# Kernel tuning notes

Measured on AMD Instinct MI355X. Metric: run time of the kernel, lower is better.

The kernel has to match this reference:

```python
import jax, jax.numpy as jnp
import numpy as np

D_MODEL = 1024
NUM_HEADS = 16
HEAD_DIM = D_MODEL // NUM_HEADS


def setup_inputs() -> dict:
    key = jax.random.key(0)
    k_x, k_wqkv, k_bqkv, k_wout, k_bout = jax.random.split(key, 5)
    B, S = 2, 2048
    x = jax.random.normal(k_x, (B, S, D_MODEL), dtype=jnp.float32)
    # haiku Linear: y = x @ W + b, W shape [in, out]
    init_scale = 1.0 / np.sqrt(D_MODEL)
    W_qkv = jax.random.normal(k_wqkv, (D_MODEL, 3 * D_MODEL), dtype=jnp.float32) * init_scale
    b_qkv = jnp.zeros((3 * D_MODEL,), dtype=jnp.float32)
    W_out = jax.random.normal(k_wout, (D_MODEL, D_MODEL), dtype=jnp.float32) * init_scale
    b_out = jnp.zeros((D_MODEL,), dtype=jnp.float32)
    return {"x": x, "W_qkv": W_qkv, "b_qkv": b_qkv, "W_out": W_out, "b_out": b_out}


def reference(x, W_qkv, b_qkv, W_out, b_out):
    B, S, _ = x.shape
    qkv = x @ W_qkv + b_qkv                      # [B, S, 3*D]
    q, k, v = jnp.split(qkv, 3, axis=-1)         # each [B, S, D]
    # [B, S, D] -> [B, H, S, Hd]
    def heads(t):
        return t.reshape(B, S, NUM_HEADS, HEAD_DIM).transpose(0, 2, 1, 3)
    q, k, v = heads(q), heads(k), heads(v)
    scale = jnp.sqrt(jnp.float32(HEAD_DIM)).astype(x.dtype)
    attn = jnp.einsum('bhqd,bhkd->bhqk', q, k) / scale   # [B, H, S, S]
    attn = jax.nn.softmax(attn, axis=-1)
    out = jnp.einsum('bhqk,bhkd->bhqd', attn, v)          # [B, H, S, Hd]
    out = out.transpose(0, 2, 1, 3).reshape(B, S, D_MODEL)
    return out @ W_out + b_out
```

## Files before the change

kernel.cpp:

```cpp
#include <hip/hip_runtime.h>
#include <stdint.h>


#define BATCH 2
#define SEQ 2048
#define DM 1024
#define NH 16
#define HD 64
#define M_TOT 4096
#define QSCALE 0.18033688011112042f

typedef __bf16 bf16x8 __attribute__((ext_vector_type(8)));
typedef __bf16 bf16x4 __attribute__((ext_vector_type(4)));
typedef float  f32x4  __attribute__((ext_vector_type(4)));

__device__ __forceinline__ void gld_lds16(const void* g, void* l) {
    __builtin_amdgcn_global_load_lds(
        (const __attribute__((address_space(1))) uint32_t*)g,
        (__attribute__((address_space(3))) uint32_t*)l, 16, 0, 0);
}

__device__ __forceinline__ int swz(int r, int c) {
    return r * 64 + ((((c >> 3) ^ (r & 7))) << 3) + (c & 7);
}

__launch_bounds__(256)
__global__ void prep_kernel(const float* __restrict__ x,
                            const float* __restrict__ Wqkv,
                            const float* __restrict__ Wout,
                            __bf16* __restrict__ xs,
                            __bf16* __restrict__ wqt,
                            __bf16* __restrict__ wot)
{
    __shared__ float T[64][69];
    const int tid = threadIdx.x;
    const int blk = blockIdx.x;

    if (blk < 4096) {
        const int i  = blk * 256 + tid;
        const int m  = i >> 8;
        const int c4 = (i & 255) * 4;
        float4 v = *reinterpret_cast<const float4*>(&x[(size_t)m * DM + c4]);
        float a[4] = {v.x, v.y, v.z, v.w};
        bf16x4 hi, lo;
        #pragma unroll
        for (int j = 0; j < 4; ++j) {
            __bf16 h = (__bf16)a[j];
            hi[j] = h;
            lo[j] = (__bf16)(a[j] - (float)h);
        }
        *reinterpret_cast<bf16x4*>(&xs[(size_t)m * (2*DM) + c4]) = hi;
        *reinterpret_cast<bf16x4*>(&xs[(size_t)m * (2*DM) + DM + c4]) = lo;
        return;
    }

    const int bb = (blk < 4864) ? blk - 4096 : blk - 4864;
    const float* W = (blk < 4864) ? Wqkv : Wout;
    __bf16* Wt     = (blk < 4864) ? wqt  : wot;
    const int N    = (blk < 4864) ? 3 * DM : DM;
    const int k0 = (bb & 15) * 64, n0 = (bb >> 4) * 64;

    {
        const int kr = tid >> 4, c4 = (tid & 15) * 4;
        #pragma unroll
        for (int i = 0; i < 4; ++i) {
            float4 v = *reinterpret_cast<const float4*>(
                &W[(size_t)(k0 + kr + 16 * i) * N + n0 + c4]);
            *reinterpret_cast<float4*>(&T[kr + 16 * i][c4]) = v;
        }
    }
    __syncthreads();
    {
        const int n = tid >> 2, kc = (tid & 3) * 16;
        __bf16 hi[16], lo[16];
        #pragma unroll
        for (int j = 0; j < 16; ++j) {
            float v = T[kc + j][n];
            __bf16 h = (__bf16)v;
            hi[j] = h;
            lo[j] = (__bf16)(v - (float)h);
        }
        const size_t ro = (size_t)(n0 + n) * (2*DM) + k0 + kc;
        *reinterpret_cast<bf16x8*>(&Wt[ro])          = *reinterpret_cast<bf16x8*>(&hi[0]);
        *reinterpret_cast<bf16x8*>(&Wt[ro + 8])      = *reinterpret_cast<bf16x8*>(&hi[8]);
        *reinterpret_cast<bf16x8*>(&Wt[ro + DM])     = *reinterpret_cast<bf16x8*>(&lo[0]);
        *reinterpret_cast<bf16x8*>(&Wt[ro + DM + 8]) = *reinterpret_cast<bf16x8*>(&lo[8]);
    }
}

__launch_bounds__(256)
__global__ void gemm_qkv_kernel(const __bf16* __restrict__ A,
                                const __bf16* __restrict__ Bt,
                                const float* __restrict__ bias,
                                __bf16* __restrict__ qs,
                                __bf16* __restrict__ khi_g,
                                __bf16* __restrict__ klo_g,
                                __bf16* __restrict__ vt_g)
{
    __shared__ __align__(16) __bf16 pool[18432];
    __bf16* AsH = pool;
    __bf16* AsL = pool + 4096;
    __bf16* BsH = pool + 8192;
    __bf16* BsL = pool + 12288;

    const int tid  = threadIdx.x;
    const int w    = tid >> 6;
    const int lane = tid & 63;
    const int n16  = lane & 15;
    const int quad = lane >> 4;
    const int bm = blockIdx.x * 128, bn = blockIdx.y * 128;
    const int wm = (w & 1) * 64,     wn = (w >> 1) * 64;

    const int srow = tid >> 2, sc = (tid & 3) * 8;
    const __bf16* Ar = A  + (size_t)(bm + srow) * (2*DM) + sc;
    const __bf16* Br = Bt + (size_t)(bn + srow) * (2*DM) + sc;

    f32x4 acc[4][4] = {};

    for (int k0 = 0; k0 < DM; k0 += 32) {
        __syncthreads();
        gld_lds16(Ar + k0,                         &AsH[(size_t)tid * 8]);
        gld_lds16(Ar + k0 + (size_t)64*2*DM,       &AsH[(size_t)(256 + tid) * 8]);
        gld_lds16(Ar + DM + k0,                    &AsL[(size_t)tid * 8]);
        gld_lds16(Ar + DM + k0 + (size_t)64*2*DM,  &AsL[(size_t)(256 + tid) * 8]);
        gld_lds16(Br + k0,                         &BsH[(size_t)tid * 8]);
        gld_lds16(Br + k0 + (size_t)64*2*DM,       &BsH[(size_t)(256 + tid) * 8]);
        gld_lds16(Br + DM + k0,                    &BsL[(size_t)tid * 8]);
        gld_lds16(Br + DM + k0 + (size_t)64*2*DM,  &BsL[(size_t)(256 + tid) * 8]);
        __syncthreads();

        bf16x8 afh[4], afl[4], bfh[4], bfl[4];
        #pragma unroll
        for (int i = 0; i < 4; ++i) {
            const int ro = (wm + i*16 + n16) * 32 + quad * 8;
            afh[i] = *reinterpret_cast<const bf16x8*>(&AsH[ro]);
            afl[i] = *reinterpret_cast<const bf16x8*>(&AsL[ro]);
        }
        #pragma unroll
        for (int j = 0; j < 4; ++j) {
            const int ro = (wn + j*16 + n16) * 32 + quad * 8;
            bfh[j] = *reinterpret_cast<const bf16x8*>(&BsH[ro]);
            bfl[j] = *reinterpret_cast<const bf16x8*>(&BsL[ro]);
        }
        #pragma unroll
        for (int i = 0; i < 4; ++i)
            #pragma unroll
            for (int j = 0; j < 4; ++j) {
                acc[i][j] = __builtin_amdgcn_mfma_f32_16x16x32_bf16(afh[i], bfh[j], acc[i][j], 0, 0, 0);
                acc[i][j] = __builtin_amdgcn_mfma_f32_16x16x32_bf16(afh[i], bfl[j], acc[i][j], 0, 0, 0);
                acc[i][j] = __builtin_amdgcn_mfma_f32_16x16x32_bf16(afl[i], bfh[j], acc[i][j], 0, 0, 0);
            }
    }

    const int colb = bn + wn;
    const int part = colb >> 10;
    const int hh   = (colb & 1023) >> 6;
    const int brow = bm + wm;
    const int b    = brow >> 11;
    const int s0   = brow & 2047;
    const int bh   = b * NH + hh;
    const int kt   = s0 >> 6;
    const size_t tb = ((size_t)bh * 32 + kt) * 4096;

    float bv[4];
    #pragma unroll
    for (int j = 0; j < 4; ++j) bv[j] = bias[colb + j * 16 + n16];

    __bf16* scrH = pool + w * 4608;
    __bf16* scrL = scrH + 2304;
    const int lr = lane & 31, hc = lane >> 5;

    __syncthreads();

    #pragma unroll
    for (int p = 0; p < 2; ++p) {
        if (part == 2) {
            #pragma unroll
            for (int jj = 0; jj < 2; ++jj) {
                const int j = 2 * p + jj;
                #pragma unroll
                for (int i = 0; i < 4; ++i) {
                    bf16x4 v4;
                    #pragma unroll
                    for (int r = 0; r < 4; ++r)
                        v4[r] = (__bf16)(acc[i][j][r] + bv[j]);
                    *reinterpret_cast<bf16x4*>(
                        &scrH[(jj * 16 + n16) * 72 + i * 16 + quad * 4]) = v4;
                }
            }
        } else {
            #pragma unroll
            for (int ii = 0; ii < 2; ++ii) {
                const int i = 2 * p + ii;
                #pragma unroll
                for (int j = 0; j < 4; ++j) {
                    #pragma unroll
                    for (int r = 0; r < 4; ++r) {
                        float val = acc[i][j][r] + bv[j];
                        if (part == 0) val *= QSCALE;
                        __bf16 h = (__bf16)val;
                        const int so = (ii * 16 + quad * 4 + r) * 72 + j * 16 + n16;
                        scrH[so] = h;
                        scrL[so] = (__bf16)(val - (float)h);
                    }
                }
            }
        }
        __syncthreads();

        if (part == 0) {
            const size_t qbase = ((size_t)bh * SEQ + s0 + 32 * p + lr) * 128;
            #pragma unroll
            for (int t = 0; t < 4; ++t) {
                const int ch = hc * 4 + t;
                *reinterpret_cast<bf16x8*>(&qs[qbase + ch * 8]) =
                    *reinterpret_cast<const bf16x8*>(&scrH[lr * 72 + ch * 8]);
                *reinterpret_cast<bf16x8*>(&qs[qbase + 64 + ch * 8]) =
                    *reinterpret_cast<const bf16x8*>(&scrL[lr * 72 + ch * 8]);
            }
        } else if (part == 1) {
            const int kr = 32 * p + lr;
            #pragma unroll
            for (int t = 0; t < 4; ++t) {
                const int ch = hc * 4 + t;
                const int src = (ch ^ (lr & 7)) * 8;
                *reinterpret_cast<bf16x8*>(&khi_g[tb + kr * 64 + ch * 8]) =
                    *reinterpret_cast<const bf16x8*>(&scrH[lr * 72 + src]);
                *reinterpret_cast<bf16x8*>(&klo_g[tb + kr * 64 + ch * 8]) =
                    *reinterpret_cast<const bf16x8*>(&scrL[lr * 72 + src]);
            }
        } else {
            const int d = 32 * p + lr;
            #pragma unroll
            for (int t = 0; t < 4; ++t) {
                const int ch = hc * 4 + t;
                const int src = (ch ^ (lr & 7)) * 8;
                *reinterpret_cast<bf16x8*>(&vt_g[tb + d * 64 + ch * 8]) =
                    *reinterpret_cast<const bf16x8*>(&scrH[lr * 72 + src]);
            }
        }
        __syncthreads();
    }
}

__launch_bounds__(256)
__global__ void gemm_out_kernel(const __bf16* __restrict__ A,
                                const __bf16* __restrict__ Bt,
                                const float* __restrict__ bias,
                                float* __restrict__ out)
{
    __shared__ __align__(16) __bf16 AsH[128 * 32];
    __shared__ __align__(16) __bf16 AsL[128 * 32];
    __shared__ __align__(16) __bf16 BsH[64 * 32];
    __shared__ __align__(16) __bf16 BsL[64 * 32];

    const int tid  = threadIdx.x;
    const int w    = tid >> 6;
    const int lane = tid & 63;
    const int n16  = lane & 15;
    const int quad = lane >> 4;
    const int bm = blockIdx.x * 128, bn = blockIdx.y * 64;
    const int wm = (w & 1) * 64,     wn = (w >> 1) * 32;

    const int srow = tid >> 2, sc = (tid & 3) * 8;
    const __bf16* Ar = A  + (size_t)(bm + srow) * (2*DM) + sc;
    const __bf16* Br = Bt + (size_t)(bn + srow) * (2*DM) + sc;

    f32x4 acc[4][2] = {};

    for (int k0 = 0; k0 < DM; k0 += 32) {
        __syncthreads();
        gld_lds16(Ar + k0,                         &AsH[(size_t)tid * 8]);
        gld_lds16(Ar + k0 + (size_t)64*2*DM,       &AsH[(size_t)(256 + tid) * 8]);
        gld_lds16(Ar + DM + k0,                    &AsL[(size_t)tid * 8]);
        gld_lds16(Ar + DM + k0 + (size_t)64*2*DM,  &AsL[(size_t)(256 + tid) * 8]);
        gld_lds16(Br + k0,                         &BsH[(size_t)tid * 8]);
        gld_lds16(Br + DM + k0,                    &BsL[(size_t)tid * 8]);
        __syncthreads();

        bf16x8 afh[4], afl[4], bfh[2], bfl[2];
        #pragma unroll
        for (int i = 0; i < 4; ++i) {
            const int ro = (wm + i*16 + n16) * 32 + quad * 8;
            afh[i] = *reinterpret_cast<const bf16x8*>(&AsH[ro]);
            afl[i] = *reinterpret_cast<const bf16x8*>(&AsL[ro]);
        }
        #pragma unroll
        for (int j = 0; j < 2; ++j) {
            const int ro = (wn + j*16 + n16) * 32 + quad * 8;
            bfh[j] = *reinterpret_cast<const bf16x8*>(&BsH[ro]);
            bfl[j] = *reinterpret_cast<const bf16x8*>(&BsL[ro]);
        }
        #pragma unroll
        for (int i = 0; i < 4; ++i)
            #pragma unroll
            for (int j = 0; j < 2; ++j) {
                acc[i][j] = __builtin_amdgcn_mfma_f32_16x16x32_bf16(afh[i], bfh[j], acc[i][j], 0, 0, 0);
                acc[i][j] = __builtin_amdgcn_mfma_f32_16x16x32_bf16(afh[i], bfl[j], acc[i][j], 0, 0, 0);
                acc[i][j] = __builtin_amdgcn_mfma_f32_16x16x32_bf16(afl[i], bfh[j], acc[i][j], 0, 0, 0);
            }
    }

    #pragma unroll
    for (int j = 0; j < 2; ++j) {
        const int col = bn + wn + j * 16 + n16;
        const float bvv = bias[col];
        #pragma unroll
        for (int i = 0; i < 4; ++i) {
            const int row0 = bm + wm + i * 16 + quad * 4;
            #pragma unroll
            for (int r = 0; r < 4; ++r)
                out[(size_t)(row0 + r) * DM + col] = acc[i][j][r] + bvv;
        }
    }
}

__launch_bounds__(256, 2)
__global__ void flash_attn_v4_kernel(const __bf16* __restrict__ qs,
                                     const __bf16* __restrict__ khi_g,
                                     const __bf16* __restrict__ klo_g,
                                     const __bf16* __restrict__ vt_g,
                                     __bf16* __restrict__ ctx2)
{
    __shared__ __align__(16) __bf16 Khi[4096];
    __shared__ __align__(16) __bf16 Klo[4096];
    __shared__ __align__(16) __bf16 Vt [4096];
    __shared__ __align__(16) __bf16 Ps [8192];

    const int tid  = threadIdx.x;
    const int w    = tid >> 6;
    const int lane = tid & 63;
    const int n16  = lane & 15;
    const int quad = lane >> 4;
    const int bid  = blockIdx.x;
    const int bh = (bid & 7) * 4 + (bid >> 7);
    const int qt = (bid >> 3) & 15;

    bf16x8 qh[2][2], ql[2][2];
    #pragma unroll
    for (int qg = 0; qg < 2; ++qg) {
        const size_t qrow =
            ((size_t)bh * SEQ + qt * 128 + w * 32 + qg * 16 + n16) * 128;
        #pragma unroll
        for (int s2 = 0; s2 < 2; ++s2) {
            qh[qg][s2] = *reinterpret_cast<const bf16x8*>(&qs[qrow + s2 * 32 + quad * 8]);
            ql[qg][s2] = *reinterpret_cast<const bf16x8*>(&qs[qrow + 64 + s2 * 32 + quad * 8]);
        }
    }

    f32x4 o[2][4] = {};
    float l_lane[2] = {};

    for (int kt = 0; kt < 32; ++kt) {
        const size_t tb = ((size_t)bh * 32 + kt) * 4096;
        __syncthreads();
        #pragma unroll
        for (int t = 0; t < 6; ++t) {
            const int ch = w * 6 + t;
            const int arr = ch >> 3, sub = ch & 7;
            const int eo = sub * 512 + lane * 8;
            const __bf16* g = (arr == 0 ? khi_g : arr == 1 ? klo_g : vt_g) + tb + eo;
            __bf16* l = (arr == 0 ? Khi : arr == 1 ? Klo : Vt) + eo;
            gld_lds16(g, l);
        }
        __syncthreads();

        #pragma unroll
        for (int kg = 0; kg < 4; ++kg) {
            const int r = kg * 16 + n16;
            const int o0 = r * 64 + ((quad ^ (r & 7)) << 3);
            const int o1 = r * 64 + (((4 + quad) ^ (r & 7)) << 3);
            bf16x8 kh0 = *reinterpret_cast<const bf16x8*>(&Khi[o0]);
            bf16x8 kl0 = *reinterpret_cast<const bf16x8*>(&Klo[o0]);
            bf16x8 kh1 = *reinterpret_cast<const bf16x8*>(&Khi[o1]);
            bf16x8 kl1 = *reinterpret_cast<const bf16x8*>(&Klo[o1]);
            #pragma unroll
            for (int qg = 0; qg < 2; ++qg) {
                f32x4 st = {};
                st = __builtin_amdgcn_mfma_f32_16x16x32_bf16(kh0, qh[qg][0], st, 0, 0, 0);
                st = __builtin_amdgcn_mfma_f32_16x16x32_bf16(kl0, qh[qg][0], st, 0, 0, 0);
                st = __builtin_amdgcn_mfma_f32_16x16x32_bf16(kh0, ql[qg][0], st, 0, 0, 0);
                st = __builtin_amdgcn_mfma_f32_16x16x32_bf16(kh1, qh[qg][1], st, 0, 0, 0);
                st = __builtin_amdgcn_mfma_f32_16x16x32_bf16(kl1, qh[qg][1], st, 0, 0, 0);
                st = __builtin_amdgcn_mfma_f32_16x16x32_bf16(kh1, ql[qg][1], st, 0, 0, 0);

                f32x4 pp;
                #pragma unroll
                for (int r2 = 0; r2 < 4; ++r2) pp[r2] = exp2f(st[r2]);
                l_lane[qg] += (pp[0] + pp[1]) + (pp[2] + pp[3]);

                bf16x4 p4;
                #pragma unroll
                for (int r2 = 0; r2 < 4; ++r2) p4[r2] = (__bf16)pp[r2];
                const int prow = w * 32 + qg * 16 + n16;
                const int ch2 = kg * 2 + (quad >> 1);
                const int off = prow * 64 + ((ch2 ^ (prow & 7)) << 3) + (quad & 1) * 4;
                *reinterpret_cast<bf16x4*>(&Ps[off]) = p4;
            }
        }

        bf16x8 pa[2][2];
        #pragma unroll
        for (int qg = 0; qg < 2; ++qg) {
            const int prow = w * 32 + qg * 16 + n16;
            #pragma unroll
            for (int s2 = 0; s2 < 2; ++s2)
                pa[qg][s2] = *reinterpret_cast<const bf16x8*>(
                    &Ps[prow * 64 + (((s2 * 4 + quad) ^ (prow & 7)) << 3)]);
        }
        #pragma unroll
        for (int c = 0; c < 4; ++c) {
            const int vr = c * 16 + n16;
            bf16x8 vb0 = *reinterpret_cast<const bf16x8*>(
                &Vt[vr * 64 + ((quad ^ (vr & 7)) << 3)]);
            bf16x8 vb1 = *reinterpret_cast<const bf16x8*>(
                &Vt[vr * 64 + (((4 + quad) ^ (vr & 7)) << 3)]);
            #pragma unroll
            for (int qg = 0; qg < 2; ++qg) {
                o[qg][c] = __builtin_amdgcn_mfma_f32_16x16x32_bf16(pa[qg][0], vb0, o[qg][c], 0, 0, 0);
                o[qg][c] = __builtin_amdgcn_mfma_f32_16x16x32_bf16(pa[qg][1], vb1, o[qg][c], 0, 0, 0);
            }
        }
    }

    #pragma unroll
    for (int qg = 0; qg < 2; ++qg) {
        l_lane[qg] += __shfl_xor(l_lane[qg], 16, 64);
        l_lane[qg] += __shfl_xor(l_lane[qg], 32, 64);
    }

    const int b = bh >> 4, hh = bh & 15;
    #pragma unroll
    for (int qg = 0; qg < 2; ++qg) {
        #pragma unroll
        for (int r2 = 0; r2 < 4; ++r2) {
            const float l = __shfl(l_lane[qg], (quad << 4) + quad * 4 + r2, 64);
            const float linv = 1.0f / l;
            const int srow = qt * 128 + w * 32 + qg * 16 + quad * 4 + r2;
            const size_t rowoff = (size_t)(b * SEQ + srow) * (2*DM);
            #pragma unroll
            for (int c = 0; c < 4; ++c) {
                const int col = hh * HD + c * 16 + n16;
                float v = o[qg][c][r2] * linv;
                __bf16 h = (__bf16)v;
                ctx2[rowoff + col] = h;
                ctx2[rowoff + DM + col] = (__bf16)(v - (float)h);
            }
        }
    }
}

extern "C" void kernel_launch(void* const* d_in, const int* in_sizes, int n_in,
                              void* d_out, int out_size, void* d_ws, size_t ws_size,
                              hipStream_t stream)
{
    const float* x    = (const float*)d_in[0];
    const float* Wqkv = (const float*)d_in[1];
    const float* bqkv = (const float*)d_in[2];
    const float* Wout = (const float*)d_in[3];
    const float* bout = (const float*)d_in[4];
    float* out = (float*)d_out;

    char* ws = (char*)d_ws;
    __bf16* xs   = (__bf16*)(ws);
    __bf16* ctx2 = xs;
    __bf16* wqt  = (__bf16*)(ws + (size_t)16 * 1024 * 1024);
    __bf16* wot  = (__bf16*)(ws + (size_t)28 * 1024 * 1024);
    __bf16* qsb  = (__bf16*)(ws + (size_t)32 * 1024 * 1024);
    __bf16* khi  = (__bf16*)(ws + (size_t)48 * 1024 * 1024);
    __bf16* klo  = (__bf16*)(ws + (size_t)56 * 1024 * 1024);
    __bf16* vt   = (__bf16*)(ws + (size_t)64 * 1024 * 1024);

    prep_kernel<<<dim3(5120), 256, 0, stream>>>(x, Wqkv, Wout, xs, wqt, wot);
    gemm_qkv_kernel<<<dim3(M_TOT / 128, (3 * DM) / 128), 256, 0, stream>>>(
        xs, wqt, bqkv, qsb, khi, klo, vt);
    flash_attn_v4_kernel<<<dim3(512), 256, 0, stream>>>(qsb, khi, klo, vt, ctx2);
    gemm_out_kernel<<<dim3(M_TOT / 128, DM / 64), 256, 0, stream>>>(
        ctx2, wot, bout, out);
}
```

Baseline: 296.4 us.

## Flatten split-bf16 QKV GEMM K-loop and process two KV tiles per attention barrier

The QKV GEMM's hi/lo split products are recast as one long K loop of 3*DM. Each step loads a single A and B tile, chosen by offset, and issues 16 MFMAs instead of 48. This cuts register pressure and LDS footprint per step but triples the number of barrier-separated iterations. The attention kernel now loads two 64-key K/V tiles per barrier pair into doubled LDS buffers, halving synchronisation count. It also splits the six-MFMA score chain into two independent accumulators to expose more MFMA parallelism, at the cost of larger LDS use per block, which may affect occupancy.

```diff
diff --git a/kernel.cpp b/kernel.cpp
--- a/kernel.cpp
+++ b/kernel.cpp
@@ -98,10 +98,8 @@
                                 __bf16* __restrict__ vt_g)
 {
     __shared__ __align__(16) __bf16 pool[18432];
-    __bf16* AsH = pool;
-    __bf16* AsL = pool + 4096;
-    __bf16* BsH = pool + 8192;
-    __bf16* BsL = pool + 12288;
+    __bf16* As = pool;
+    __bf16* Bs = pool + 4096;
 
     const int tid  = threadIdx.x;
     const int w    = tid >> 6;
@@ -117,39 +115,28 @@
 
     f32x4 acc[4][4] = {};
 
-    for (int k0 = 0; k0 < DM; k0 += 32) {
-        __syncthreads();
-        gld_lds16(Ar + k0,                         &AsH[(size_t)tid * 8]);
-        gld_lds16(Ar + k0 + (size_t)64*2*DM,       &AsH[(size_t)(256 + tid) * 8]);
-        gld_lds16(Ar + DM + k0,                    &AsL[(size_t)tid * 8]);
-        gld_lds16(Ar + DM + k0 + (size_t)64*2*DM,  &AsL[(size_t)(256 + tid) * 8]);
-        gld_lds16(Br + k0,                         &BsH[(size_t)tid * 8]);
-        gld_lds16(Br + k0 + (size_t)64*2*DM,       &BsH[(size_t)(256 + tid) * 8]);
-        gld_lds16(Br + DM + k0,                    &BsL[(size_t)tid * 8]);
-        gld_lds16(Br + DM + k0 + (size_t)64*2*DM,  &BsL[(size_t)(256 + tid) * 8]);
-        __syncthreads();
-
-        bf16x8 afh[4], afl[4], bfh[4], bfl[4];
-        #pragma unroll
-        for (int i = 0; i < 4; ++i) {
-            const int ro = (wm + i*16 + n16) * 32 + quad * 8;
-            afh[i] = *reinterpret_cast<const bf16x8*>(&AsH[ro]);
-            afl[i] = *reinterpret_cast<const bf16x8*>(&AsL[ro]);
-        }
-        #pragma unroll
-        for (int j = 0; j < 4; ++j) {
-            const int ro = (wn + j*16 + n16) * 32 + quad * 8;
-            bfh[j] = *reinterpret_cast<const bf16x8*>(&BsH[ro]);
-            bfl[j] = *reinterpret_cast<const bf16x8*>(&BsL[ro]);
-        }
+    for (int kb = 0; kb < 3 * DM; kb += 32) {
+        const int a_k = (kb < DM)     ? kb : kb - DM;
+        const int b_k = (kb < 2 * DM) ? kb : kb - 2 * DM;
+        __syncthreads();
+        gld_lds16(Ar + a_k,                    &As[(size_t)tid * 8]);
+        gld_lds16(Ar + a_k + (size_t)64*2*DM,  &As[(size_t)(256 + tid) * 8]);
+        gld_lds16(Br + b_k,                    &Bs[(size_t)tid * 8]);
+        gld_lds16(Br + b_k + (size_t)64*2*DM,  &Bs[(size_t)(256 + tid) * 8]);
+        __syncthreads();
+
+        bf16x8 af[4], bfr[4];
         #pragma unroll
         for (int i = 0; i < 4; ++i)
-            #pragma unroll
-            for (int j = 0; j < 4; ++j) {
-                acc[i][j] = __builtin_amdgcn_mfma_f32_16x16x32_bf16(afh[i], bfh[j], acc[i][j], 0, 0, 0);
-                acc[i][j] = __builtin_amdgcn_mfma_f32_16x16x32_bf16(afh[i], bfl[j], acc[i][j], 0, 0, 0);
-                acc[i][j] = __builtin_amdgcn_mfma_f32_16x16x32_bf16(afl[i], bfh[j], acc[i][j], 0, 0, 0);
-            }
+            af[i] = *reinterpret_cast<const bf16x8*>(&As[(wm + i*16 + n16) * 32 + quad * 8]);
+        #pragma unroll
+        for (int j = 0; j < 4; ++j)
+            bfr[j] = *reinterpret_cast<const bf16x8*>(&Bs[(wn + j*16 + n16) * 32 + quad * 8]);
+        #pragma unroll
+        for (int i = 0; i < 4; ++i)
+            #pragma unroll
+            for (int j = 0; j < 4; ++j)
+                acc[i][j] = __builtin_amdgcn_mfma_f32_16x16x32_bf16(af[i], bfr[j], acc[i][j], 0, 0, 0);
     }
 
     const int colb = bn + wn;
@@ -316,15 +303,15 @@
 }
 
 __launch_bounds__(256, 2)
-__global__ void flash_attn_v4_kernel(const __bf16* __restrict__ qs,
+__global__ void flash_attn_v5_kernel(const __bf16* __restrict__ qs,
                                      const __bf16* __restrict__ khi_g,
                                      const __bf16* __restrict__ klo_g,
                                      const __bf16* __restrict__ vt_g,
                                      __bf16* __restrict__ ctx2)
 {
-    __shared__ __align__(16) __bf16 Khi[4096];
-    __shared__ __align__(16) __bf16 Klo[4096];
-    __shared__ __align__(16) __bf16 Vt [4096];
+    __shared__ __align__(16) __bf16 Khi[2][4096];
+    __shared__ __align__(16) __bf16 Klo[2][4096];
+    __shared__ __align__(16) __bf16 Vt [2][4096];
     __shared__ __align__(16) __bf16 Ps [8192];
 
     const int tid  = threadIdx.x;
@@ -351,74 +338,85 @@
     f32x4 o[2][4] = {};
     float l_lane[2] = {};
 
-    for (int kt = 0; kt < 32; ++kt) {
-        const size_t tb = ((size_t)bh * 32 + kt) * 4096;
-        __syncthreads();
-        #pragma unroll
-        for (int t = 0; t < 6; ++t) {
-            const int ch = w * 6 + t;
-            const int arr = ch >> 3, sub = ch & 7;
-            const int eo = sub * 512 + lane * 8;
-            const __bf16* g = (arr == 0 ? khi_g : arr == 1 ? klo_g : vt_g) + tb + eo;
-            __bf16* l = (arr == 0 ? Khi : arr == 1 ? Klo : Vt) + eo;
-            gld_lds16(g, l);
-        }
-        __syncthreads();
-
-        #pragma unroll
-        for (int kg = 0; kg < 4; ++kg) {
-            const int r = kg * 16 + n16;
-            const int o0 = r * 64 + ((quad ^ (r & 7)) << 3);
-            const int o1 = r * 64 + (((4 + quad) ^ (r & 7)) << 3);
-            bf16x8 kh0 = *reinterpret_cast<const bf16x8*>(&Khi[o0]);
-            bf16x8 kl0 = *reinterpret_cast<const bf16x8*>(&Klo[o0]);
-            bf16x8 kh1 = *reinterpret_cast<const bf16x8*>(&Khi[o1]);
-            bf16x8 kl1 = *reinterpret_cast<const bf16x8*>(&Klo[o1]);
+    for (int kt2 = 0; kt2 < 16; ++kt2) {
+        __syncthreads();
+        {
+            const int buf = w >> 1;
+            const size_t tb = ((size_t)bh * 32 + kt2 * 2 + buf) * 4096;
+            #pragma unroll
+            for (int t = 0; t < 12; ++t) {
+                const int rem = (w & 1) * 12 + t;
+                const int arr = rem >> 3, sub = rem & 7;
+                const int eo = sub * 512 + lane * 8;
+                const __bf16* g = (arr == 0 ? khi_g : arr == 1 ? klo_g : vt_g) + tb + eo;
+                __bf16* l = (arr == 0 ? Khi[buf] : arr == 1 ? Klo[buf] : Vt[buf]) + eo;
+                gld_lds16(g, l);
+            }
+        }
+        __syncthreads();
+
+        #pragma unroll
+        for (int hf = 0; hf < 2; ++hf) {
+            const __bf16* KhiB = Khi[hf];
+            const __bf16* KloB = Klo[hf];
+            const __bf16* VtB  = Vt[hf];
+
+            #pragma unroll
+            for (int kg = 0; kg < 4; ++kg) {
+                const int r = kg * 16 + n16;
+                const int o0 = r * 64 + ((quad ^ (r & 7)) << 3);
+                const int o1 = r * 64 + (((4 + quad) ^ (r & 7)) << 3);
+                bf16x8 kh0 = *reinterpret_cast<const bf16x8*>(&KhiB[o0]);
+                bf16x8 kl0 = *reinterpret_cast<const bf16x8*>(&KloB[o0]);
+                bf16x8 kh1 = *reinterpret_cast<const bf16x8*>(&KhiB[o1]);
+                bf16x8 kl1 = *reinterpret_cast<const bf16x8*>(&KloB[o1]);
+                #pragma unroll
+                for (int qg = 0; qg < 2; ++qg) {
+                    f32x4 sa = {}, sb = {};
+                    sa = __builtin_amdgcn_mfma_f32_16x16x32_bf16(kh0, qh[qg][0], sa, 0, 0, 0);
+                    sb = __builtin_amdgcn_mfma_f32_16x16x32_bf16(kh1, qh[qg][1], sb, 0, 0, 0);
+                    sa = __builtin_amdgcn_mfma_f32_16x16x32_bf16(kl0, qh[qg][0], sa, 0, 0, 0);
+                    sb = __builtin_amdgcn_mfma_f32_16x16x32_bf16(kl1, qh[qg][1], sb, 0, 0, 0);
+                    sa = __builtin_amdgcn_mfma_f32_16x16x32_bf16(kh0, ql[qg][0], sa, 0, 0, 0);
+                    sb = __builtin_amdgcn_mfma_f32_16x16x32_bf16(kh1, ql[qg][1], sb, 0, 0, 0);
+                    f32x4 st = sa + sb;
+
+                    f32x4 pp;
+                    #pragma unroll
+                    for (int r2 = 0; r2 < 4; ++r2) pp[r2] = exp2f(st[r2]);
+                    l_lane[qg] += (pp[0] + pp[1]) + (pp[2] + pp[3]);
+
+                    bf16x4 p4;
+                    #pragma unroll
+                    for (int r2 = 0; r2 < 4; ++r2) p4[r2] = (__bf16)pp[r2];
+                    const int prow = w * 32 + qg * 16 + n16;
+                    const int ch2 = kg * 2 + (quad >> 1);
+                    const int off = prow * 64 + ((ch2 ^ (prow & 7)) << 3) + (quad & 1) * 4;
+                    *reinterpret_cast<bf16x4*>(&Ps[off]) = p4;
+                }
+            }
+
+            bf16x8 pa[2][2];
             #pragma unroll
             for (int qg = 0; qg < 2; ++qg) {
-                f32x4 st = {};
-                st = __builtin_amdgcn_mfma_f32_16x16x32_bf16(kh0, qh[qg][0], st, 0, 0, 0);
-                st = __builtin_amdgcn_mfma_f32_16x16x32_bf16(kl0, qh[qg][0], st, 0, 0, 0);
-                st = __builtin_amdgcn_mfma_f32_16x16x32_bf16(kh0, ql[qg][0], st, 0, 0, 0);
-                st = __builtin_amdgcn_mfma_f32_16x16x32_bf16(kh1, qh[qg][1], st, 0, 0, 0);
-                st = __builtin_amdgcn_mfma_f32_16x16x32_bf16(kl1, qh[qg][1], st, 0, 0, 0);
-                st = __builtin_amdgcn_mfma_f32_16x16x32_bf16(kh1, ql[qg][1], st, 0, 0, 0);
-
-                f32x4 pp;
+                const int prow = w * 32 + qg * 16 + n16;
                 #pragma unroll
-                for (int r2 = 0; r2 < 4; ++r2) pp[r2] = exp2f(st[r2]);
-                l_lane[qg] += (pp[0] + pp[1]) + (pp[2] + pp[3]);
-
-                bf16x4 p4;
+                for (int s2 = 0; s2 < 2; ++s2)
+                    pa[qg][s2] = *reinterpret_cast<const bf16x8*>(
+                        &Ps[prow * 64 + (((s2 * 4 + quad) ^ (prow & 7)) << 3)]);
+            }
+            #pragma unroll
+            for (int c = 0; c < 4; ++c) {
+                const int vr = c * 16 + n16;
+                bf16x8 vb0 = *reinterpret_cast<const bf16x8*>(
+                    &VtB[vr * 64 + ((quad ^ (vr & 7)) << 3)]);
+                bf16x8 vb1 = *reinterpret_cast<const bf16x8*>(
+                    &VtB[vr * 64 + (((4 + quad) ^ (vr & 7)) << 3)]);
                 #pragma unroll
-                for (int r2 = 0; r2 < 4; ++r2) p4[r2] = (__bf16)pp[r2];
-                const int prow = w * 32 + qg * 16 + n16;
-                const int ch2 = kg * 2 + (quad >> 1);
-                const int off = prow * 64 + ((ch2 ^ (prow & 7)) << 3) + (quad & 1) * 4;
-                *reinterpret_cast<bf16x4*>(&Ps[off]) = p4;
-            }
-        }
-
-        bf16x8 pa[2][2];
-        #pragma unroll
-        for (int qg = 0; qg < 2; ++qg) {
-            const int prow = w * 32 + qg * 16 + n16;
-            #pragma unroll
-            for (int s2 = 0; s2 < 2; ++s2)
-                pa[qg][s2] = *reinterpret_cast<const bf16x8*>(
-                    &Ps[prow * 64 + (((s2 * 4 + quad) ^ (prow & 7)) << 3)]);
-        }
-        #pragma unroll
-        for (int c = 0; c < 4; ++c) {
-            const int vr = c * 16 + n16;
-            bf16x8 vb0 = *reinterpret_cast<const bf16x8*>(
-                &Vt[vr * 64 + ((quad ^ (vr & 7)) << 3)]);
-            bf16x8 vb1 = *reinterpret_cast<const bf16x8*>(
-                &Vt[vr * 64 + (((4 + quad) ^ (vr & 7)) << 3)]);
-            #pragma unroll
-            for (int qg = 0; qg < 2; ++qg) {
-                o[qg][c] = __builtin_amdgcn_mfma_f32_16x16x32_bf16(pa[qg][0], vb0, o[qg][c], 0, 0, 0);
-                o[qg][c] = __builtin_amdgcn_mfma_f32_16x16x32_bf16(pa[qg][1], vb1, o[qg][c], 0, 0, 0);
+                for (int qg = 0; qg < 2; ++qg) {
+                    o[qg][c] = __builtin_amdgcn_mfma_f32_16x16x32_bf16(pa[qg][0], vb0, o[qg][c], 0, 0, 0);
+                    o[qg][c] = __builtin_amdgcn_mfma_f32_16x16x32_bf16(pa[qg][1], vb1, o[qg][c], 0, 0, 0);
+                }
             }
         }
     }
@@ -474,7 +472,7 @@
     prep_kernel<<<dim3(5120), 256, 0, stream>>>(x, Wqkv, Wout, xs, wqt, wot);
     gemm_qkv_kernel<<<dim3(M_TOT / 128, (3 * DM) / 128), 256, 0, stream>>>(
         xs, wqt, bqkv, qsb, khi, klo, vt);
-    flash_attn_v4_kernel<<<dim3(512), 256, 0, stream>>>(qsb, khi, klo, vt, ctx2);
+    flash_attn_v5_kernel<<<dim3(512), 256, 0, stream>>>(qsb, khi, klo, vt, ctx2);
     gemm_out_kernel<<<dim3(M_TOT / 128, DM / 64), 256, 0, stream>>>(
         ctx2, wot, bout, out);
 }
```

After: 295.6 us. About the same (-0.3%).
